# Performance work log

Hardware: AMD Instinct MI355X
Metric: run time of the kernel (lower is better)

Reference implementation:

```python
import jax, jax.numpy as jnp
import numpy as np
import math

T, B, N, D = 4, 4, 1024, 512
H = 8
HD = D // H
EPS = 1e-6


def setup_inputs() -> dict:
    key = jax.random.key(0)
    ks = jax.random.split(key, 9)
    s = 1.0 / math.sqrt(D)
    inp = {"x": jax.random.normal(ks[0], (T, B, N, D), dtype=jnp.float32)}
    names = ["wq", "wk", "wv", "wo"]
    for i, nm in enumerate(names):
        inp[nm] = jax.random.uniform(ks[1 + i], (D, D), dtype=jnp.float32, minval=-s, maxval=s)
        inp["b" + nm[1]] = jax.random.uniform(ks[5 + i], (D,), dtype=jnp.float32, minval=-s, maxval=s)
    return inp


def reference(x, wq, bq, wk, bk, wv, bv, wo, bo):
    t, b, n, d = x.shape
    # torch Linear: y = x @ W.T + bias
    q = x @ wq.T + bq
    k = x @ wk.T + bk
    v = x @ wv.T + bv
    # (t, b, n, H, HD) -> (t, b, H, n, HD)
    qh = q.reshape(t, b, n, H, HD).transpose(0, 1, 3, 2, 4)
    kh = k.reshape(t, b, n, H, HD).transpose(0, 1, 3, 2, 4)
    vh = v.reshape(t, b, n, H, HD).transpose(0, 1, 3, 2, 4)
    scores = jnp.einsum("tbhqd,tbhkd->tbhqk", qh, kh) / math.sqrt(HD)
    attn = jax.nn.relu(scores)
    attn = attn / (attn.sum(axis=-1, keepdims=True) + EPS)
    ctx = jnp.einsum("tbhqk,tbhkd->tbhqd", attn, vh)
    out = ctx.transpose(0, 1, 3, 2, 4).reshape(t, b, n, d)
    return out @ wo.T + bo
```

## Files before the change

### kernel.cpp

```cpp
#include <hip/hip_runtime.h>

typedef unsigned short u16;
typedef __attribute__((ext_vector_type(8))) short bf16x8;
typedef __attribute__((ext_vector_type(4))) float f32x4;
typedef __attribute__((ext_vector_type(16))) float f32x16;
typedef __attribute__((ext_vector_type(2))) unsigned int u32x2;

__device__ inline u16 f2b(float f) {
    unsigned u;
    __builtin_memcpy(&u, &f, 4);
    unsigned r = u + 0x7FFF + ((u >> 16) & 1);
    return (u16)(r >> 16);
}

__device__ inline bf16x8 pack8(const float* p) {
    union { u16 us[8]; bf16x8 v; } r;
#pragma unroll
    for (int i = 0; i < 8; i++) r.us[i] = f2b(p[i]);
    return r.v;
}

__device__ inline unsigned cvtpk(float lo, float hi) {
    unsigned r;
    asm("v_cvt_pk_bf16_f32 %0, %1, %2" : "=v"(r) : "v"(lo), "v"(hi));
    return r;
}

__device__ inline void gload16(const void* g, void* l) {
    __builtin_amdgcn_global_load_lds((__attribute__((address_space(1))) void*)g,
                                     (__attribute__((address_space(3))) void*)l, 16, 0, 0);
}

__global__ __launch_bounds__(256) void conv_kernel(const float* __restrict__ x,
                                                   const float* __restrict__ wq,
                                                   const float* __restrict__ wk,
                                                   const float* __restrict__ wv,
                                                   const float* __restrict__ wo,
                                                   u16* __restrict__ xb, u16* __restrict__ wb) {
    const int bid = blockIdx.x;
    const float* src;
    u16* dst;
    size_t base;
    if (bid < 4096) {
        src = x; dst = xb; base = (size_t)bid * 2048;
    } else {
        const int wsel = (bid - 4096) >> 7;
        src = (wsel == 0) ? wq : (wsel == 1) ? wk : (wsel == 2) ? wv : wo;
        dst = wb + (size_t)wsel * 262144;
        base = (size_t)((bid - 4096) & 127) * 2048;
    }
    const size_t idx = base + (size_t)threadIdx.x * 8;
    float a[8];
    *(float4*)&a[0] = *(const float4*)&src[idx];
    *(float4*)&a[4] = *(const float4*)&src[idx + 4];
    *(bf16x8*)&dst[idx] = pack8(a);
}

template <int MODE>
__global__ __launch_bounds__(256) void gemm_kernel(const u16* __restrict__ A,
                                                   const u16* __restrict__ W,
                                                   const float* __restrict__ B0,
                                                   const float* __restrict__ B1,
                                                   const float* __restrict__ B2,
                                                   void* __restrict__ O0v, u16* __restrict__ O1,
                                                   u16* __restrict__ O2) {
    const int m0 = blockIdx.x * 128;
    const int n0 = blockIdx.y * 128;
    const int seg = (MODE == 0) ? (n0 >> 9) : 0;
    const int nl0 = (MODE == 0) ? (n0 & 511) : n0;
    const float* Bb = (seg == 0) ? B0 : (seg == 1) ? B1 : B2;
    u16* O = (seg == 0) ? (u16*)O0v : (seg == 1) ? O1 : O2;

    __shared__ __align__(16) u16 Al[2][128 * 64];
    __shared__ __align__(16) u16 Bl[2][128 * 64];

    const int tid = threadIdx.x;
    const int lane = tid & 63, wave = tid >> 6;
    const int quad = lane >> 4, col = lane & 15;
    const int wm = wave >> 1, wn = wave & 1;

    int srow[4], ssc[4];
#pragma unroll
    for (int i = 0; i < 4; i++) {
        const int cl = tid + i * 256;
        srow[i] = cl >> 3;
        ssc[i] = ((cl & 7) ^ (srow[i] & 7)) * 8;
    }
    const int c7 = col & 7;

#define GSTAGE(BUF, K0)                                                                     \
    {                                                                                       \
        _Pragma("unroll") for (int i_ = 0; i_ < 4; i_++) {                                  \
            const int cl_ = tid + i_ * 256;                                                 \
            gload16(&A[(size_t)(m0 + srow[i_]) * 512 + (K0) + ssc[i_]], &Al[BUF][cl_ * 8]); \
        }                                                                                   \
        _Pragma("unroll") for (int i_ = 0; i_ < 4; i_++) {                                  \
            const int cl_ = tid + i_ * 256;                                                 \
            gload16(&W[(size_t)(n0 + srow[i_]) * 512 + (K0) + ssc[i_]], &Bl[BUF][cl_ * 8]); \
        }                                                                                   \
    }

    f32x4 acc[4][4];
#pragma unroll
    for (int i = 0; i < 4; i++)
#pragma unroll
        for (int j = 0; j < 4; j++) acc[i][j] = (f32x4){0.f, 0.f, 0.f, 0.f};

    GSTAGE(0, 0)
    __syncthreads();

    int bufi = 0;
    for (int k0 = 0; k0 < 512; k0 += 64) {
        if (k0 < 448) GSTAGE(bufi ^ 1, k0 + 64)

#pragma unroll
        for (int kk = 0; kk < 2; kk++) {
            bf16x8 af[4], bfr[4];
#pragma unroll
            for (int t = 0; t < 4; t++) {
                af[t] = *(const bf16x8*)&Al[bufi][((wm * 64 + t * 16 + col) * 8 +
                                                  ((kk * 4 + quad) ^ c7)) * 8];
                bfr[t] = *(const bf16x8*)&Bl[bufi][((wn * 64 + t * 16 + col) * 8 +
                                                    ((kk * 4 + quad) ^ c7)) * 8];
            }
            __builtin_amdgcn_s_setprio(1);
#pragma unroll
            for (int i = 0; i < 4; i++)
#pragma unroll
                for (int j = 0; j < 4; j++)
                    acc[i][j] =
                        __builtin_amdgcn_mfma_f32_16x16x32_bf16(af[i], bfr[j], acc[i][j], 0, 0, 0);
            __builtin_amdgcn_s_setprio(0);
        }
        __syncthreads();
        bufi ^= 1;
    }
#undef GSTAGE

    float bias[4];
#pragma unroll
    for (int j = 0; j < 4; j++) bias[j] = Bb[nl0 + wn * 64 + j * 16 + col];

#pragma unroll
    for (int i = 0; i < 4; i++) {
        const int mbase = m0 + wm * 64 + i * 16 + quad * 4;
#pragma unroll
        for (int j = 0; j < 4; j++) {
            const int nl = nl0 + wn * 64 + j * 16 + col;
            if (MODE == 1) {
                float* Of = (float*)O0v;
#pragma unroll
                for (int r = 0; r < 4; r++)
                    Of[(size_t)(mbase + r) * 512 + nl] = acc[i][j][r] + bias[j];
            } else {
                const int h = nl >> 6, hd = nl & 63;
                if (seg < 2) {
                    const float qs = (seg == 0) ? 0.125f : 1.f;
#pragma unroll
                    for (int r = 0; r < 4; r++) {
                        int m = mbase + r;
                        int s = m >> 10, tok = m & 1023;
                        O[(size_t)((s * 8 + h) * 1024 + tok) * 64 + hd] =
                            f2b((acc[i][j][r] + bias[j]) * qs);
                    }
                } else {
                    int s = mbase >> 10, tok0 = mbase & 1023;
                    union { u16 us[4]; uint2 v; } pk;
#pragma unroll
                    for (int r = 0; r < 4; r++) pk.us[r] = f2b(acc[i][j][r] + bias[j]);
                    *(uint2*)&O[(size_t)((s * 8 + h) * 64 + hd) * 1024 + tok0] = pk.v;
                }
            }
        }
    }
}

__global__ __launch_bounds__(256, 2) void attn_kernel(const u16* __restrict__ Q,
                                                      const u16* __restrict__ Kp,
                                                      const u16* __restrict__ Vt,
                                                      u16* __restrict__ Ctx) {
    __shared__ __align__(16) u16 Kl[2][8192];
    __shared__ __align__(16) u16 Vl[2][8192];

    const int bid = blockIdx.x;
    const int head = bid & 127;
    const int qt = bid >> 7;
    const int s = head >> 3, h = head & 7;
    const u16* Qh = Q + (size_t)head * 65536;
    const u16* Kh = Kp + (size_t)head * 65536;
    const u16* Vh = Vt + (size_t)head * 65536;

    const int tid = threadIdx.x;
    const int lane = tid & 63, wave = tid >> 6;
    const int l31 = lane & 31, hi = lane >> 5;
    const int q0 = qt * 256 + wave * 64;
    const int cx = l31 & 7;

    int offK[4], offV[4];
#pragma unroll
    for (int i = 0; i < 4; i++) {
        const int p = tid + i * 256;
        const int kr = p >> 3, kc = (p & 7) ^ (kr & 7);
        offK[i] = kr * 64 + kc * 8;
        const int vr = p >> 4, vc = (p & 15) ^ (vr & 7);
        offV[i] = vr * 1024 + vc * 8;
    }

#define STAGE(B, K0)                                                            \
    {                                                                           \
        _Pragma("unroll") for (int i_ = 0; i_ < 4; i_++) {                      \
            const int p_ = tid + i_ * 256;                                      \
            gload16(&Kh[(size_t)(K0) * 64 + offK[i_]], &Kl[B][p_ * 8]);         \
        }                                                                       \
        _Pragma("unroll") for (int i_ = 0; i_ < 4; i_++) {                      \
            const int p_ = tid + i_ * 256;                                      \
            gload16(&Vh[(size_t)(K0) + offV[i_]], &Vl[B][p_ * 8]);              \
        }                                                                       \
    }

    union { u16 us[8]; bf16x8 v; } one;
#pragma unroll
    for (int i = 0; i < 8; i++) one.us[i] = 0x3F80;
    const bf16x8 onesf = one.v;

    f32x16 zf;
#pragma unroll
    for (int r = 0; r < 16; r++) zf[r] = 0.f;

    bf16x8 qf[2][4];
#pragma unroll
    for (int q2 = 0; q2 < 2; q2++)
#pragma unroll
        for (int kk = 0; kk < 4; kk++)
            qf[q2][kk] =
                *(const bf16x8*)&Qh[(size_t)(q0 + q2 * 32 + l31) * 64 + kk * 16 + hi * 8];

    f32x16 cacc[2][2];
    f32x16 dacc[2];
#pragma unroll
    for (int q2 = 0; q2 < 2; q2++) {
#pragma unroll
        for (int r = 0; r < 16; r++) {
            cacc[q2][0][r] = 0.f;
            cacc[q2][1][r] = 0.f;
            dacc[q2][r] = 0.f;
        }
    }

    STAGE(0, 0)
    __syncthreads();

    int buf = 0;
    for (int kt = 0; kt < 8; kt++) {
        if (kt < 7) STAGE(buf ^ 1, (kt + 1) * 128)

#pragma unroll
        for (int mt = 0; mt < 4; mt++) {
            f32x16 s0, s1;
            __builtin_amdgcn_s_setprio(1);
#pragma unroll
            for (int kk = 0; kk < 4; kk++) {
                const bf16x8 kf =
                    *(const bf16x8*)&Kl[buf][((mt * 32 + l31) * 8 + ((2 * kk + hi) ^ cx)) * 8];
                s0 = __builtin_amdgcn_mfma_f32_32x32x16_bf16(kf, qf[0][kk], kk ? s0 : zf, 0, 0, 0);
                s1 = __builtin_amdgcn_mfma_f32_32x32x16_bf16(kf, qf[1][kk], kk ? s1 : zf, 0, 0, 0);
            }
            __builtin_amdgcn_s_setprio(0);

            bf16x8 paq[2][2];
#pragma unroll
            for (int q2 = 0; q2 < 2; q2++) {
                const f32x16& sc = q2 ? s1 : s0;
                const unsigned c0 = cvtpk(fmaxf(sc[0], 0.f), fmaxf(sc[1], 0.f));
                const unsigned c1 = cvtpk(fmaxf(sc[2], 0.f), fmaxf(sc[3], 0.f));
                const unsigned c2 = cvtpk(fmaxf(sc[4], 0.f), fmaxf(sc[5], 0.f));
                const unsigned c3 = cvtpk(fmaxf(sc[6], 0.f), fmaxf(sc[7], 0.f));
                const unsigned c4 = cvtpk(fmaxf(sc[8], 0.f), fmaxf(sc[9], 0.f));
                const unsigned c5 = cvtpk(fmaxf(sc[10], 0.f), fmaxf(sc[11], 0.f));
                const unsigned c6 = cvtpk(fmaxf(sc[12], 0.f), fmaxf(sc[13], 0.f));
                const unsigned c7 = cvtpk(fmaxf(sc[14], 0.f), fmaxf(sc[15], 0.f));
                const u32x2 s02 = __builtin_amdgcn_permlane32_swap(c0, c2, false, false);
                const u32x2 s13 = __builtin_amdgcn_permlane32_swap(c1, c3, false, false);
                const u32x2 s46 = __builtin_amdgcn_permlane32_swap(c4, c6, false, false);
                const u32x2 s57 = __builtin_amdgcn_permlane32_swap(c5, c7, false, false);
                union { unsigned u[4]; bf16x8 v; } f0u, f1u;
                f0u.u[0] = s02.x; f0u.u[1] = s13.x; f0u.u[2] = s02.y; f0u.u[3] = s13.y;
                f1u.u[0] = s46.x; f1u.u[1] = s57.x; f1u.u[2] = s46.y; f1u.u[3] = s57.y;
                paq[q2][0] = f0u.v;
                paq[q2][1] = f1u.v;
            }

            const bf16x8 vfa0 = *(const bf16x8*)&Vl[buf][(l31 * 16 + ((4 * mt + hi) ^ cx)) * 8];
            const bf16x8 vfa1 =
                *(const bf16x8*)&Vl[buf][((32 + l31) * 16 + ((4 * mt + hi) ^ cx)) * 8];
            const bf16x8 vfb0 =
                *(const bf16x8*)&Vl[buf][(l31 * 16 + ((4 * mt + 2 + hi) ^ cx)) * 8];
            const bf16x8 vfb1 =
                *(const bf16x8*)&Vl[buf][((32 + l31) * 16 + ((4 * mt + 2 + hi) ^ cx)) * 8];
            __builtin_amdgcn_s_setprio(1);
            dacc[0] = __builtin_amdgcn_mfma_f32_32x32x16_bf16(paq[0][0], onesf, dacc[0], 0, 0, 0);
            cacc[0][0] = __builtin_amdgcn_mfma_f32_32x32x16_bf16(paq[0][0], vfa0, cacc[0][0], 0, 0, 0);
            cacc[0][1] = __builtin_amdgcn_mfma_f32_32x32x16_bf16(paq[0][0], vfa1, cacc[0][1], 0, 0, 0);
            dacc[1] = __builtin_amdgcn_mfma_f32_32x32x16_bf16(paq[1][0], onesf, dacc[1], 0, 0, 0);
            cacc[1][0] = __builtin_amdgcn_mfma_f32_32x32x16_bf16(paq[1][0], vfa0, cacc[1][0], 0, 0, 0);
            cacc[1][1] = __builtin_amdgcn_mfma_f32_32x32x16_bf16(paq[1][0], vfa1, cacc[1][1], 0, 0, 0);
            dacc[0] = __builtin_amdgcn_mfma_f32_32x32x16_bf16(paq[0][1], onesf, dacc[0], 0, 0, 0);
            cacc[0][0] = __builtin_amdgcn_mfma_f32_32x32x16_bf16(paq[0][1], vfb0, cacc[0][0], 0, 0, 0);
            cacc[0][1] = __builtin_amdgcn_mfma_f32_32x32x16_bf16(paq[0][1], vfb1, cacc[0][1], 0, 0, 0);
            dacc[1] = __builtin_amdgcn_mfma_f32_32x32x16_bf16(paq[1][1], onesf, dacc[1], 0, 0, 0);
            cacc[1][0] = __builtin_amdgcn_mfma_f32_32x32x16_bf16(paq[1][1], vfb0, cacc[1][0], 0, 0, 0);
            cacc[1][1] = __builtin_amdgcn_mfma_f32_32x32x16_bf16(paq[1][1], vfb1, cacc[1][1], 0, 0, 0);
            __builtin_amdgcn_s_setprio(0);
        }

        __syncthreads();
        buf ^= 1;
    }
#undef STAGE

#pragma unroll
    for (int q2 = 0; q2 < 2; q2++) {
#pragma unroll
        for (int r = 0; r < 16; r++) {
            const int ql = (r & 3) + 8 * (r >> 2) + 4 * hi;
            const float inv = 1.f / (dacc[q2][r] + 1e-6f);
            const size_t grow = (size_t)(s * 1024 + q0 + q2 * 32 + ql);
            Ctx[grow * 512 + h * 64 + l31] = f2b(cacc[q2][0][r] * inv);
            Ctx[grow * 512 + h * 64 + 32 + l31] = f2b(cacc[q2][1][r] * inv);
        }
    }
}

extern "C" void kernel_launch(void* const* d_in, const int* in_sizes, int n_in, void* d_out,
                              int out_size, void* d_ws, size_t ws_size, hipStream_t stream) {
    const float* x = (const float*)d_in[0];
    const float* wq = (const float*)d_in[1];
    const float* bq = (const float*)d_in[2];
    const float* wk = (const float*)d_in[3];
    const float* bk = (const float*)d_in[4];
    const float* wv = (const float*)d_in[5];
    const float* bv = (const float*)d_in[6];
    const float* wo = (const float*)d_in[7];
    const float* bo = (const float*)d_in[8];

    const size_t E = 16384ull * 512ull;
    u16* xb = (u16*)d_ws;
    u16* cw = xb;
    u16* wb = xb + E;
    u16* qw = wb + 4 * 262144;
    u16* kw = qw + E;
    u16* vw = kw + E;

    conv_kernel<<<dim3(4096 + 512), 256, 0, stream>>>(x, wq, wk, wv, wo, xb, wb);
    gemm_kernel<0><<<dim3(128, 12), 256, 0, stream>>>(xb, wb, bq, bk, bv, qw, kw, vw);
    attn_kernel<<<dim3(512), 256, 0, stream>>>(qw, kw, vw, cw);
    gemm_kernel<1><<<dim3(128, 4), 256, 0, stream>>>(cw, wb + 3 * 262144, bo, nullptr, nullptr,
                                                     d_out, nullptr, nullptr);
}
```

Before: 185.2 us.

## Fuse fp32-to-bf16 conversion of x into QKV GEMM A-tile staging

```diff
diff --git a/kernel.cpp b/kernel.cpp
--- a/kernel.cpp
+++ b/kernel.cpp
@@ -31,25 +31,16 @@
                                      (__attribute__((address_space(3))) void*)l, 16, 0, 0);
 }
 
-__global__ __launch_bounds__(256) void conv_kernel(const float* __restrict__ x,
-                                                   const float* __restrict__ wq,
+__global__ __launch_bounds__(256) void conv_kernel(const float* __restrict__ wq,
                                                    const float* __restrict__ wk,
                                                    const float* __restrict__ wv,
                                                    const float* __restrict__ wo,
-                                                   u16* __restrict__ xb, u16* __restrict__ wb) {
+                                                   u16* __restrict__ wb) {
     const int bid = blockIdx.x;
-    const float* src;
-    u16* dst;
-    size_t base;
-    if (bid < 4096) {
-        src = x; dst = xb; base = (size_t)bid * 2048;
-    } else {
-        const int wsel = (bid - 4096) >> 7;
-        src = (wsel == 0) ? wq : (wsel == 1) ? wk : (wsel == 2) ? wv : wo;
-        dst = wb + (size_t)wsel * 262144;
-        base = (size_t)((bid - 4096) & 127) * 2048;
-    }
-    const size_t idx = base + (size_t)threadIdx.x * 8;
+    const int wsel = bid >> 7;
+    const float* src = (wsel == 0) ? wq : (wsel == 1) ? wk : (wsel == 2) ? wv : wo;
+    u16* dst = wb + (size_t)wsel * 262144;
+    const size_t idx = (size_t)(bid & 127) * 2048 + (size_t)threadIdx.x * 8;
     float a[8];
     *(float4*)&a[0] = *(const float4*)&src[idx];
     *(float4*)&a[4] = *(const float4*)&src[idx + 4];
@@ -57,13 +48,15 @@
 }
 
 template <int MODE>
-__global__ __launch_bounds__(256) void gemm_kernel(const u16* __restrict__ A,
+__global__ __launch_bounds__(256) void gemm_kernel(const void* __restrict__ Av,
                                                    const u16* __restrict__ W,
                                                    const float* __restrict__ B0,
                                                    const float* __restrict__ B1,
                                                    const float* __restrict__ B2,
                                                    void* __restrict__ O0v, u16* __restrict__ O1,
                                                    u16* __restrict__ O2) {
+    const float* Af = (const float*)Av;
+    const u16* Ab = (const u16*)Av;
     const int m0 = blockIdx.x * 128;
     const int n0 = blockIdx.y * 128;
     const int seg = (MODE == 0) ? (n0 >> 9) : 0;
@@ -88,17 +81,42 @@
     }
     const int c7 = col & 7;
 
-#define GSTAGE(BUF, K0)                                                                     \
+#define GSTAGE_W(BUF, K0)                                                                   \
     {                                                                                       \
-        _Pragma("unroll") for (int i_ = 0; i_ < 4; i_++) {                                  \
-            const int cl_ = tid + i_ * 256;                                                 \
-            gload16(&A[(size_t)(m0 + srow[i_]) * 512 + (K0) + ssc[i_]], &Al[BUF][cl_ * 8]); \
-        }                                                                                   \
         _Pragma("unroll") for (int i_ = 0; i_ < 4; i_++) {                                  \
             const int cl_ = tid + i_ * 256;                                                 \
             gload16(&W[(size_t)(n0 + srow[i_]) * 512 + (K0) + ssc[i_]], &Bl[BUF][cl_ * 8]); \
         }                                                                                   \
     }
+#define GSTAGE_A(BUF, K0)                                                                    \
+    {                                                                                        \
+        _Pragma("unroll") for (int i_ = 0; i_ < 4; i_++) {                                   \
+            const int cl_ = tid + i_ * 256;                                                  \
+            gload16(&Ab[(size_t)(m0 + srow[i_]) * 512 + (K0) + ssc[i_]], &Al[BUF][cl_ * 8]); \
+        }                                                                                    \
+    }
+#define ASTAGE_LOAD(K0)                                                          \
+    {                                                                            \
+        _Pragma("unroll") for (int i_ = 0; i_ < 4; i_++) {                       \
+            const float* ap_ = &Af[(size_t)(m0 + srow[i_]) * 512 + (K0) + ssc[i_]]; \
+            pfa[i_][0] = *(const float4*)ap_;                                    \
+            pfa[i_][1] = *(const float4*)(ap_ + 4);                              \
+        }                                                                        \
+    }
+#define ASTAGE_WRITE(BUF)                                                        \
+    {                                                                            \
+        _Pragma("unroll") for (int i_ = 0; i_ < 4; i_++) {                       \
+            const int cl_ = tid + i_ * 256;                                      \
+            union { unsigned u[4]; bf16x8 v; } wpk_;                             \
+            wpk_.u[0] = cvtpk(pfa[i_][0].x, pfa[i_][0].y);                       \
+            wpk_.u[1] = cvtpk(pfa[i_][0].z, pfa[i_][0].w);                       \
+            wpk_.u[2] = cvtpk(pfa[i_][1].x, pfa[i_][1].y);                       \
+            wpk_.u[3] = cvtpk(pfa[i_][1].z, pfa[i_][1].w);                       \
+            *(bf16x8*)&Al[BUF][cl_ * 8] = wpk_.v;                                \
+        }                                                                        \
+    }
+
+    float4 pfa[4][2];
 
     f32x4 acc[4][4];
 #pragma unroll
@@ -106,12 +124,23 @@
 #pragma unroll
         for (int j = 0; j < 4; j++) acc[i][j] = (f32x4){0.f, 0.f, 0.f, 0.f};
 
-    GSTAGE(0, 0)
+    if constexpr (MODE == 0) {
+        ASTAGE_LOAD(0)
+        ASTAGE_WRITE(0)
+        GSTAGE_W(0, 0)
+    } else {
+        GSTAGE_A(0, 0)
+        GSTAGE_W(0, 0)
+    }
     __syncthreads();
 
     int bufi = 0;
     for (int k0 = 0; k0 < 512; k0 += 64) {
-        if (k0 < 448) GSTAGE(bufi ^ 1, k0 + 64)
+        if (k0 < 448) {
+            if constexpr (MODE == 0) ASTAGE_LOAD(k0 + 64)
+            else GSTAGE_A(bufi ^ 1, k0 + 64)
+            GSTAGE_W(bufi ^ 1, k0 + 64)
+        }
 
 #pragma unroll
         for (int kk = 0; kk < 2; kk++) {
@@ -132,10 +161,17 @@
                         __builtin_amdgcn_mfma_f32_16x16x32_bf16(af[i], bfr[j], acc[i][j], 0, 0, 0);
             __builtin_amdgcn_s_setprio(0);
         }
+
+        if constexpr (MODE == 0) {
+            if (k0 < 448) ASTAGE_WRITE(bufi ^ 1)
+        }
         __syncthreads();
         bufi ^= 1;
     }
-#undef GSTAGE
+#undef GSTAGE_W
+#undef GSTAGE_A
+#undef ASTAGE_LOAD
+#undef ASTAGE_WRITE
 
     float bias[4];
 #pragma unroll
@@ -223,10 +259,6 @@
     for (int i = 0; i < 8; i++) one.us[i] = 0x3F80;
     const bf16x8 onesf = one.v;
 
-    f32x16 zf;
-#pragma unroll
-    for (int r = 0; r < 16; r++) zf[r] = 0.f;
-
     bf16x8 qf[2][4];
 #pragma unroll
     for (int q2 = 0; q2 < 2; q2++)
@@ -257,13 +289,15 @@
 #pragma unroll
         for (int mt = 0; mt < 4; mt++) {
             f32x16 s0, s1;
+#pragma unroll
+            for (int r = 0; r < 16; r++) { s0[r] = 0.f; s1[r] = 0.f; }
             __builtin_amdgcn_s_setprio(1);
 #pragma unroll
             for (int kk = 0; kk < 4; kk++) {
                 const bf16x8 kf =
                     *(const bf16x8*)&Kl[buf][((mt * 32 + l31) * 8 + ((2 * kk + hi) ^ cx)) * 8];
-                s0 = __builtin_amdgcn_mfma_f32_32x32x16_bf16(kf, qf[0][kk], kk ? s0 : zf, 0, 0, 0);
-                s1 = __builtin_amdgcn_mfma_f32_32x32x16_bf16(kf, qf[1][kk], kk ? s1 : zf, 0, 0, 0);
+                s0 = __builtin_amdgcn_mfma_f32_32x32x16_bf16(kf, qf[0][kk], s0, 0, 0, 0);
+                s1 = __builtin_amdgcn_mfma_f32_32x32x16_bf16(kf, qf[1][kk], s1, 0, 0, 0);
             }
             __builtin_amdgcn_s_setprio(0);
 
@@ -344,16 +378,15 @@
     const float* bo = (const float*)d_in[8];
 
     const size_t E = 16384ull * 512ull;
-    u16* xb = (u16*)d_ws;
-    u16* cw = xb;
-    u16* wb = xb + E;
+    u16* cw = (u16*)d_ws;
+    u16* wb = cw + E;
     u16* qw = wb + 4 * 262144;
     u16* kw = qw + E;
     u16* vw = kw + E;
 
-    conv_kernel<<<dim3(4096 + 512), 256, 0, stream>>>(x, wq, wk, wv, wo, xb, wb);
-    gemm_kernel<0><<<dim3(128, 12), 256, 0, stream>>>(xb, wb, bq, bk, bv, qw, kw, vw);
-    attn_kernel<<<dim3(512), 256, 0, stream>>>(qw, kw, vw, cw);
+    conv_kernel<<<dim3(512), 256, 0, stream>>>(wq, wk, wv, wo, wb);
+    gemm_kernel<0><<<dim3(128, 12), 256, 0, stream>>>(x, wb, bq, bk, bv, qw, kw, vw);
+    attn_kernel<<<dim3(1024 >> 1), 256, 0, stream>>>(qw, kw, vw, cw);
     gemm_kernel<1><<<dim3(128, 4), 256, 0, stream>>>(cw, wb + 3 * 262144, bo, nullptr, nullptr,
                                                      d_out, nullptr, nullptr);
 }
```

New measurement: 198.6 us. +7.2%, slower.
